# Kernel tuning notes

Measured on AMD Instinct MI355X. Metric: run time of the kernel, lower is better.

## Reference

```python
import jax, jax.numpy as jnp
import numpy as np

B, IN, H = 4096, 2048, 2048

def hard_sigmoid(x):
    # torch nn.Hardsigmoid / QHardSigmoid: clip(x/6 + 0.5, 0, 1)
    return jnp.clip(x / 6.0 + 0.5, 0.0, 1.0)

def hard_tanh(x):
    return jnp.clip(x, -1.0, 1.0)

def setup_inputs() -> dict:
    key = jax.random.key(0)
    k1, k2, k3, k4, k5 = jax.random.split(key, 5)
    return {
        "input_": jax.random.normal(k1, (B, IN), dtype=jnp.float32),
        "h_0": jax.random.normal(k2, (B, H), dtype=jnp.float32),
        "c_0": jax.random.normal(k3, (B, H), dtype=jnp.float32),
        "W_ih": jax.random.normal(k4, (4 * H, IN), dtype=jnp.float32) * (1.0 / np.sqrt(IN)),
        "W_hh": jax.random.normal(k5, (4 * H, H), dtype=jnp.float32) * (1.0 / np.sqrt(H)),
        "b_hh": jnp.zeros((4 * H,), dtype=jnp.float32),
    }

def reference(input_, h_0, c_0, W_ih, W_hh, b_hh):
    # Two GEMMs: x @ W_ih^T (no bias) and h @ W_hh^T + b
    wi = jnp.einsum('bi,gi->bg', input_, W_ih)          # [B, 4H]
    wh_b = jnp.einsum('bh,gh->bg', h_0, W_hh) + b_hh     # [B, 4H]
    h_x4 = wh_b + wi
    f, i, o, g = jnp.split(h_x4, 4, axis=1)              # split order: f, i, o, g
    new = hard_sigmoid(i) * hard_tanh(g)
    old = hard_sigmoid(f) * c_0
    c_1 = old + new
    h_1 = hard_sigmoid(o) * hard_tanh(c_1)
    return (h_1, c_1)
```

## Files before the change

kernel.cpp:

```cpp
#include <hip/hip_runtime.h>
#include <hip/hip_bf16.h>


typedef __attribute__((ext_vector_type(8))) short short8;
typedef __attribute__((ext_vector_type(4))) float f32x4;

#define B_SZ 4096
#define K_SZ 4096
#define N_SZ 8192
#define H_SZ 2048

typedef const __attribute__((address_space(1))) void gvoid_t;
typedef __attribute__((address_space(3))) void lvoid_t;

__device__ __forceinline__ void gload_lds16(const __hip_bfloat16* g, void* l) {
    __builtin_amdgcn_global_load_lds((gvoid_t*)g, (lvoid_t*)l, 16, 0, 0);
}

__device__ __forceinline__ float hsig(float x) {
    return fminf(fmaxf(x * (1.0f / 6.0f) + 0.5f, 0.0f), 1.0f);
}
__device__ __forceinline__ float htanh(float x) {
    return fminf(fmaxf(x, -1.0f), 1.0f);
}

__global__ void cvt_concat_kernel(const float* __restrict__ a,
                                  const float* __restrict__ b,
                                  __hip_bfloat16* __restrict__ out,
                                  int total4)
{
    int i = blockIdx.x * blockDim.x + threadIdx.x;
    if (i >= total4) return;
    int idx = i << 2;
    int r = idx >> 12;
    int c = idx & 4095;
    const float* src = (c < 2048) ? (a + (size_t)r * 2048 + c)
                                  : (b + (size_t)r * 2048 + (c - 2048));
    float4 v = *reinterpret_cast<const float4*>(src);
    union { ushort4 u; __hip_bfloat16 h[4]; } p;
    p.h[0] = __float2bfloat16(v.x);
    p.h[1] = __float2bfloat16(v.y);
    p.h[2] = __float2bfloat16(v.z);
    p.h[3] = __float2bfloat16(v.w);
    *reinterpret_cast<ushort4*>(out + idx) = p.u;
}

__global__ void cvt_w_perm_kernel(const float* __restrict__ wih,
                                  const float* __restrict__ whh,
                                  __hip_bfloat16* __restrict__ out,
                                  int total4)
{
    int i = blockIdx.x * blockDim.x + threadIdx.x;
    if (i >= total4) return;
    int idx = i << 2;
    int r = idx >> 12;
    int c = idx & 4095;
    int gate = (((r >> 7) & 1) << 1) | ((r >> 4) & 1);
    int j = (r & 15) | (((r >> 5) & 3) << 4) | ((r >> 8) << 6);
    int srow = gate * 2048 + j;
    const float* src = (c < 2048) ? (wih + (size_t)srow * 2048 + c)
                                  : (whh + (size_t)srow * 2048 + (c - 2048));
    float4 v = *reinterpret_cast<const float4*>(src);
    union { ushort4 u; __hip_bfloat16 h[4]; } p;
    p.h[0] = __float2bfloat16(v.x);
    p.h[1] = __float2bfloat16(v.y);
    p.h[2] = __float2bfloat16(v.z);
    p.h[3] = __float2bfloat16(v.w);
    *reinterpret_cast<ushort4*>(out + idx) = p.u;
}

__global__ __launch_bounds__(512, 2)
void gemm_fused_kernel(const __hip_bfloat16* __restrict__ A,
                       const __hip_bfloat16* __restrict__ Bw,
                       const float* __restrict__ c0,
                       const float* __restrict__ bias,
                       float* __restrict__ out)
{
    constexpr int BK = 64;
    constexpr int NT = K_SZ / BK;
    constexpr int NWG = (B_SZ / 256) * (N_SZ / 256);
    constexpr int TILEB = 65536;

    extern __shared__ __align__(16) char lds[];

    const int tid  = threadIdx.x;
    const int wave = tid >> 6;
    const int lane = tid & 63;
    const int wrow = wave >> 2;
    const int wcol = wave & 3;
    const int fr   = lane & 15;
    const int fkq  = lane >> 4;

    int bid = blockIdx.x;
    int swz = (bid & 7) * (NWG / 8) + (bid >> 3);
    int bm = swz >> 5;
    int bn = swz & 31;

    const int rs  = tid >> 3;
    const int ch  = tid & 7;
    const int lch = ch ^ (rs & 7);
    const __hip_bfloat16* pa = A  + (size_t)(bm * 256 + rs) * K_SZ + lch * 8;
    const __hip_bfloat16* pb = Bw + (size_t)(bn * 256 + rs) * K_SZ + lch * 8;

#define STG_A(bufn, kt, srow) \
    gload_lds16(pa + (size_t)(srow) * K_SZ + (kt), (bufn) + (srow) * 128 + wave * 1024)
#define STG_B(bufn, kt, srow) \
    gload_lds16(pb + (size_t)(srow) * K_SZ + (kt), (bufn) + 32768 + (srow) * 128 + wave * 1024)

    int a_off[4], b_off[2];
#pragma unroll
    for (int mf = 0; mf < 4; ++mf) {
        int row = wrow * 64 + mf * 16 + fr;
        a_off[mf] = row * 128 + ((fkq ^ (row & 7)) << 4);
    }
#pragma unroll
    for (int nf = 0; nf < 2; ++nf) {
        int row = wcol * 32 + nf * 16 + fr;
        b_off[nf] = row * 128 + ((fkq ^ (row & 7)) << 4);
    }

    f32x4 acc[8][4];
#pragma unroll
    for (int m = 0; m < 8; ++m)
#pragma unroll
        for (int n = 0; n < 4; ++n)
            acc[m][n] = f32x4{0.f, 0.f, 0.f, 0.f};

    {
        char* b0 = lds;
        STG_A(b0, 0, 0);   STG_A(b0, 0, 64);
        STG_B(b0, 0, 0);   STG_B(b0, 0, 64);
        STG_A(b0, 0, 128); STG_A(b0, 0, 192);
        STG_B(b0, 0, 128); STG_B(b0, 0, 192);
    }
    asm volatile("s_waitcnt vmcnt(4)" ::: "memory");
    asm volatile("s_barrier" ::: "memory");

    short8 av[4][2], bv[2][2];

#pragma unroll 1
    for (int t = 0; t < NT; ++t) {
        char* bufc = lds + (t & 1) * TILEB;
        char* bufn = lds + ((t + 1) & 1) * TILEB;
        const char* Ab = bufc;
        const char* Bb = bufc + 32768;
        const int ktn = (t + 1) * BK;
        const bool st = (t + 1 < NT);

#pragma unroll
        for (int mf = 0; mf < 4; ++mf)
#pragma unroll
            for (int ks = 0; ks < 2; ++ks)
                av[mf][ks] = *(const short8*)(Ab + (a_off[mf] ^ (ks << 6)));
#pragma unroll
        for (int nf = 0; nf < 2; ++nf)
#pragma unroll
            for (int ks = 0; ks < 2; ++ks)
                bv[nf][ks] = *(const short8*)(Bb + (b_off[nf] ^ (ks << 6)));
        if (st) { STG_A(bufn, ktn, 0); STG_A(bufn, ktn, 64); }
        asm volatile("s_barrier" ::: "memory");
        asm volatile("s_waitcnt lgkmcnt(0)" ::: "memory");
        __builtin_amdgcn_sched_barrier(0);
        __builtin_amdgcn_s_setprio(1);
#pragma unroll
        for (int mf = 0; mf < 4; ++mf)
#pragma unroll
            for (int nf = 0; nf < 2; ++nf)
#pragma unroll
                for (int ks = 0; ks < 2; ++ks)
                    acc[mf][nf] = __builtin_amdgcn_mfma_f32_16x16x32_bf16(av[mf][ks], bv[nf][ks], acc[mf][nf], 0, 0, 0);
        __builtin_amdgcn_s_setprio(0);
        if (st) asm volatile("s_waitcnt vmcnt(2)" ::: "memory");
        else    asm volatile("s_waitcnt vmcnt(0)" ::: "memory");
        asm volatile("s_barrier" ::: "memory");

#pragma unroll
        for (int nf = 0; nf < 2; ++nf)
#pragma unroll
            for (int ks = 0; ks < 2; ++ks)
                bv[nf][ks] = *(const short8*)(Bb + 16384 + (b_off[nf] ^ (ks << 6)));
        if (st) { STG_B(bufn, ktn, 0); STG_B(bufn, ktn, 64); }
        asm volatile("s_barrier" ::: "memory");
        asm volatile("s_waitcnt lgkmcnt(0)" ::: "memory");
        __builtin_amdgcn_sched_barrier(0);
        __builtin_amdgcn_s_setprio(1);
#pragma unroll
        for (int mf = 0; mf < 4; ++mf)
#pragma unroll
            for (int nf = 0; nf < 2; ++nf)
#pragma unroll
                for (int ks = 0; ks < 2; ++ks)
                    acc[mf][2 + nf] = __builtin_amdgcn_mfma_f32_16x16x32_bf16(av[mf][ks], bv[nf][ks], acc[mf][2 + nf], 0, 0, 0);
        __builtin_amdgcn_s_setprio(0);
        asm volatile("s_barrier" ::: "memory");

#pragma unroll
        for (int mf = 0; mf < 4; ++mf)
#pragma unroll
            for (int ks = 0; ks < 2; ++ks)
                av[mf][ks] = *(const short8*)(Ab + 16384 + (a_off[mf] ^ (ks << 6)));
#pragma unroll
        for (int nf = 0; nf < 2; ++nf)
#pragma unroll
            for (int ks = 0; ks < 2; ++ks)
                bv[nf][ks] = *(const short8*)(Bb + (b_off[nf] ^ (ks << 6)));
        if (st) { STG_A(bufn, ktn, 128); STG_A(bufn, ktn, 192); }
        asm volatile("s_barrier" ::: "memory");
        asm volatile("s_waitcnt lgkmcnt(0)" ::: "memory");
        __builtin_amdgcn_sched_barrier(0);
        __builtin_amdgcn_s_setprio(1);
#pragma unroll
        for (int mf = 0; mf < 4; ++mf)
#pragma unroll
            for (int nf = 0; nf < 2; ++nf)
#pragma unroll
                for (int ks = 0; ks < 2; ++ks)
                    acc[4 + mf][nf] = __builtin_amdgcn_mfma_f32_16x16x32_bf16(av[mf][ks], bv[nf][ks], acc[4 + mf][nf], 0, 0, 0);
        __builtin_amdgcn_s_setprio(0);
        asm volatile("s_barrier" ::: "memory");

#pragma unroll
        for (int nf = 0; nf < 2; ++nf)
#pragma unroll
            for (int ks = 0; ks < 2; ++ks)
                bv[nf][ks] = *(const short8*)(Bb + 16384 + (b_off[nf] ^ (ks << 6)));
        if (st) { STG_B(bufn, ktn, 128); STG_B(bufn, ktn, 192); }
        asm volatile("s_barrier" ::: "memory");
        asm volatile("s_waitcnt lgkmcnt(0)" ::: "memory");
        __builtin_amdgcn_sched_barrier(0);
        __builtin_amdgcn_s_setprio(1);
#pragma unroll
        for (int mf = 0; mf < 4; ++mf)
#pragma unroll
            for (int nf = 0; nf < 2; ++nf)
#pragma unroll
                for (int ks = 0; ks < 2; ++ks)
                    acc[4 + mf][2 + nf] = __builtin_amdgcn_mfma_f32_16x16x32_bf16(av[mf][ks], bv[nf][ks], acc[4 + mf][2 + nf], 0, 0, 0);
        __builtin_amdgcn_s_setprio(0);
        if (st) asm volatile("s_waitcnt vmcnt(4)" ::: "memory");
        asm volatile("s_barrier" ::: "memory");
    }
#undef STG_A
#undef STG_B

    const int jj = bn * 64 + wcol * 16 + fr;
    const float bf = bias[jj];
    const float bi = bias[2048 + jj];
    const float bo = bias[4096 + jj];
    const float bg = bias[6144 + jj];
    float* h1out = out;
    float* c1out = out + (size_t)B_SZ * H_SZ;
#pragma unroll
    for (int mh = 0; mh < 2; ++mh)
#pragma unroll
        for (int mf = 0; mf < 4; ++mf) {
            const int m = mh * 4 + mf;
            const int row0 = bm * 256 + mh * 128 + wrow * 64 + mf * 16 + fkq * 4;
#pragma unroll
            for (int i = 0; i < 4; ++i) {
                int r = row0 + i;
                float c0v = c0[(size_t)r * H_SZ + jj];
                float f  = acc[m][0][i] + bf;
                float ig = acc[m][1][i] + bi;
                float o  = acc[m][2][i] + bo;
                float g  = acc[m][3][i] + bg;
                float cn = hsig(f) * c0v + hsig(ig) * htanh(g);
                h1out[(size_t)r * H_SZ + jj] = hsig(o) * htanh(cn);
                c1out[(size_t)r * H_SZ + jj] = cn;
            }
        }
}

extern "C" void kernel_launch(void* const* d_in, const int* in_sizes, int n_in,
                              void* d_out, int out_size, void* d_ws, size_t ws_size,
                              hipStream_t stream)
{
    const float* x   = (const float*)d_in[0];
    const float* h0  = (const float*)d_in[1];
    const float* c0  = (const float*)d_in[2];
    const float* Wih = (const float*)d_in[3];
    const float* Whh = (const float*)d_in[4];
    const float* bhh = (const float*)d_in[5];
    float* out = (float*)d_out;

    if (ws_size < (size_t)96 * 1024 * 1024) return;
    char* ws = (char*)d_ws;
    __hip_bfloat16* Xp = (__hip_bfloat16*)ws;
    __hip_bfloat16* Wp = (__hip_bfloat16*)(ws + (size_t)32 * 1024 * 1024);

    int t4x = B_SZ * K_SZ / 4;
    cvt_concat_kernel<<<t4x / 256, 256, 0, stream>>>(x, h0, Xp, t4x);
    int t4w = N_SZ * K_SZ / 4;
    cvt_w_perm_kernel<<<t4w / 256, 256, 0, stream>>>(Wih, Whh, Wp, t4w);

    gemm_fused_kernel<<<512, 512, 131072, stream>>>(Xp, Wp, c0, bhh, out);
}
```

Before: 480.4 us.

## Keep both B sub-tiles in registers per k-step and widen bf16 conversion to 8 elements

The GEMM main loop now loads both halves of the B tile into separate register sets (bv0, bv1) once per k-step. It reuses them across the two A halves, so the repeated B reads from LDS go away and only one A reload remains. The global-to-LDS staging order and the vmcnt wait counts are rearranged to match, and some lgkmcnt waits are dropped. The conversion kernels now process 8 floats per thread with 16-byte stores. The extra B registers raise register pressure, and the loosened waits make correctness depend on the exact order of outstanding loads.

```diff
diff --git a/kernel.cpp b/kernel.cpp
--- a/kernel.cpp
+++ b/kernel.cpp
@@ -24,35 +24,40 @@
     return fminf(fmaxf(x, -1.0f), 1.0f);
 }
 
+__device__ __forceinline__ void cvt8_store(const float* src, __hip_bfloat16* dst) {
+    float4 v0 = *reinterpret_cast<const float4*>(src);
+    float4 v1 = *reinterpret_cast<const float4*>(src + 4);
+    union { __hip_bfloat16 h[8]; uint4 q; } p;
+    p.h[0] = __float2bfloat16(v0.x); p.h[1] = __float2bfloat16(v0.y);
+    p.h[2] = __float2bfloat16(v0.z); p.h[3] = __float2bfloat16(v0.w);
+    p.h[4] = __float2bfloat16(v1.x); p.h[5] = __float2bfloat16(v1.y);
+    p.h[6] = __float2bfloat16(v1.z); p.h[7] = __float2bfloat16(v1.w);
+    *reinterpret_cast<uint4*>(dst) = p.q;
+}
+
 __global__ void cvt_concat_kernel(const float* __restrict__ a,
                                   const float* __restrict__ b,
                                   __hip_bfloat16* __restrict__ out,
-                                  int total4)
+                                  int total8)
 {
     int i = blockIdx.x * blockDim.x + threadIdx.x;
-    if (i >= total4) return;
-    int idx = i << 2;
+    if (i >= total8) return;
+    int idx = i << 3;
     int r = idx >> 12;
     int c = idx & 4095;
     const float* src = (c < 2048) ? (a + (size_t)r * 2048 + c)
                                   : (b + (size_t)r * 2048 + (c - 2048));
-    float4 v = *reinterpret_cast<const float4*>(src);
-    union { ushort4 u; __hip_bfloat16 h[4]; } p;
-    p.h[0] = __float2bfloat16(v.x);
-    p.h[1] = __float2bfloat16(v.y);
-    p.h[2] = __float2bfloat16(v.z);
-    p.h[3] = __float2bfloat16(v.w);
-    *reinterpret_cast<ushort4*>(out + idx) = p.u;
+    cvt8_store(src, out + idx);
 }
 
 __global__ void cvt_w_perm_kernel(const float* __restrict__ wih,
                                   const float* __restrict__ whh,
                                   __hip_bfloat16* __restrict__ out,
-                                  int total4)
+                                  int total8)
 {
     int i = blockIdx.x * blockDim.x + threadIdx.x;
-    if (i >= total4) return;
-    int idx = i << 2;
+    if (i >= total8) return;
+    int idx = i << 3;
     int r = idx >> 12;
     int c = idx & 4095;
     int gate = (((r >> 7) & 1) << 1) | ((r >> 4) & 1);
@@ -60,13 +65,7 @@
     int srow = gate * 2048 + j;
     const float* src = (c < 2048) ? (wih + (size_t)srow * 2048 + c)
                                   : (whh + (size_t)srow * 2048 + (c - 2048));
-    float4 v = *reinterpret_cast<const float4*>(src);
-    union { ushort4 u; __hip_bfloat16 h[4]; } p;
-    p.h[0] = __float2bfloat16(v.x);
-    p.h[1] = __float2bfloat16(v.y);
-    p.h[2] = __float2bfloat16(v.z);
-    p.h[3] = __float2bfloat16(v.w);
-    *reinterpret_cast<ushort4*>(out + idx) = p.u;
+    cvt8_store(src, out + idx);
 }
 
 __global__ __launch_bounds__(512, 2)
@@ -130,13 +129,13 @@
         char* b0 = lds;
         STG_A(b0, 0, 0);   STG_A(b0, 0, 64);
         STG_B(b0, 0, 0);   STG_B(b0, 0, 64);
+        STG_B(b0, 0, 128); STG_B(b0, 0, 192);
         STG_A(b0, 0, 128); STG_A(b0, 0, 192);
-        STG_B(b0, 0, 128); STG_B(b0, 0, 192);
-    }
-    asm volatile("s_waitcnt vmcnt(4)" ::: "memory");
+    }
+    asm volatile("s_waitcnt vmcnt(2)" ::: "memory");
     asm volatile("s_barrier" ::: "memory");
 
-    short8 av[4][2], bv[2][2];
+    short8 av[4][2], bv0[2][2], bv1[2][2];
 
 #pragma unroll 1
     for (int t = 0; t < NT; ++t) {
@@ -155,8 +154,10 @@
 #pragma unroll
         for (int nf = 0; nf < 2; ++nf)
 #pragma unroll
-            for (int ks = 0; ks < 2; ++ks)
-                bv[nf][ks] = *(const short8*)(Bb + (b_off[nf] ^ (ks << 6)));
+            for (int ks = 0; ks < 2; ++ks) {
+                bv0[nf][ks] = *(const short8*)(Bb + (b_off[nf] ^ (ks << 6)));
+                bv1[nf][ks] = *(const short8*)(Bb + 16384 + (b_off[nf] ^ (ks << 6)));
+            }
         if (st) { STG_A(bufn, ktn, 0); STG_A(bufn, ktn, 64); }
         asm volatile("s_barrier" ::: "memory");
         asm volatile("s_waitcnt lgkmcnt(0)" ::: "memory");
@@ -168,18 +169,31 @@
             for (int nf = 0; nf < 2; ++nf)
 #pragma unroll
                 for (int ks = 0; ks < 2; ++ks)
-                    acc[mf][nf] = __builtin_amdgcn_mfma_f32_16x16x32_bf16(av[mf][ks], bv[nf][ks], acc[mf][nf], 0, 0, 0);
-        __builtin_amdgcn_s_setprio(0);
-        if (st) asm volatile("s_waitcnt vmcnt(2)" ::: "memory");
+                    acc[mf][nf] = __builtin_amdgcn_mfma_f32_16x16x32_bf16(av[mf][ks], bv0[nf][ks], acc[mf][nf], 0, 0, 0);
+        __builtin_amdgcn_s_setprio(0);
+        asm volatile("s_barrier" ::: "memory");
+
+        if (st) { STG_B(bufn, ktn, 0); STG_B(bufn, ktn, 64); }
+        asm volatile("s_barrier" ::: "memory");
+        __builtin_amdgcn_s_setprio(1);
+#pragma unroll
+        for (int mf = 0; mf < 4; ++mf)
+#pragma unroll
+            for (int nf = 0; nf < 2; ++nf)
+#pragma unroll
+                for (int ks = 0; ks < 2; ++ks)
+                    acc[mf][2 + nf] = __builtin_amdgcn_mfma_f32_16x16x32_bf16(av[mf][ks], bv1[nf][ks], acc[mf][2 + nf], 0, 0, 0);
+        __builtin_amdgcn_s_setprio(0);
+        if (st) asm volatile("s_waitcnt vmcnt(4)" ::: "memory");
         else    asm volatile("s_waitcnt vmcnt(0)" ::: "memory");
         asm volatile("s_barrier" ::: "memory");
 
 #pragma unroll
-        for (int nf = 0; nf < 2; ++nf)
+        for (int mf = 0; mf < 4; ++mf)
 #pragma unroll
             for (int ks = 0; ks < 2; ++ks)
-                bv[nf][ks] = *(const short8*)(Bb + 16384 + (b_off[nf] ^ (ks << 6)));
-        if (st) { STG_B(bufn, ktn, 0); STG_B(bufn, ktn, 64); }
+                av[mf][ks] = *(const short8*)(Ab + 16384 + (a_off[mf] ^ (ks << 6)));
+        if (st) { STG_B(bufn, ktn, 128); STG_B(bufn, ktn, 192); }
         asm volatile("s_barrier" ::: "memory");
         asm volatile("s_waitcnt lgkmcnt(0)" ::: "memory");
         __builtin_amdgcn_sched_barrier(0);
@@ -190,54 +204,22 @@
             for (int nf = 0; nf < 2; ++nf)
 #pragma unroll
                 for (int ks = 0; ks < 2; ++ks)
-                    acc[mf][2 + nf] = __builtin_amdgcn_mfma_f32_16x16x32_bf16(av[mf][ks], bv[nf][ks], acc[mf][2 + nf], 0, 0, 0);
-        __builtin_amdgcn_s_setprio(0);
-        asm volatile("s_barrier" ::: "memory");
-
-#pragma unroll
-        for (int mf = 0; mf < 4; ++mf)
-#pragma unroll
-            for (int ks = 0; ks < 2; ++ks)
-                av[mf][ks] = *(const short8*)(Ab + 16384 + (a_off[mf] ^ (ks << 6)));
-#pragma unroll
-        for (int nf = 0; nf < 2; ++nf)
-#pragma unroll
-            for (int ks = 0; ks < 2; ++ks)
-                bv[nf][ks] = *(const short8*)(Bb + (b_off[nf] ^ (ks << 6)));
+                    acc[4 + mf][nf] = __builtin_amdgcn_mfma_f32_16x16x32_bf16(av[mf][ks], bv0[nf][ks], acc[4 + mf][nf], 0, 0, 0);
+        __builtin_amdgcn_s_setprio(0);
+        asm volatile("s_barrier" ::: "memory");
+
         if (st) { STG_A(bufn, ktn, 128); STG_A(bufn, ktn, 192); }
         asm volatile("s_barrier" ::: "memory");
-        asm volatile("s_waitcnt lgkmcnt(0)" ::: "memory");
-        __builtin_amdgcn_sched_barrier(0);
-        __builtin_amdgcn_s_setprio(1);
-#pragma unroll
-        for (int mf = 0; mf < 4; ++mf)
-#pragma unroll
-            for (int nf = 0; nf < 2; ++nf)
-#pragma unroll
-                for (int ks = 0; ks < 2; ++ks)
-                    acc[4 + mf][nf] = __builtin_amdgcn_mfma_f32_16x16x32_bf16(av[mf][ks], bv[nf][ks], acc[4 + mf][nf], 0, 0, 0);
-        __builtin_amdgcn_s_setprio(0);
-        asm volatile("s_barrier" ::: "memory");
-
-#pragma unroll
-        for (int nf = 0; nf < 2; ++nf)
-#pragma unroll
-            for (int ks = 0; ks < 2; ++ks)
-                bv[nf][ks] = *(const short8*)(Bb + 16384 + (b_off[nf] ^ (ks << 6)));
-        if (st) { STG_B(bufn, ktn, 128); STG_B(bufn, ktn, 192); }
-        asm volatile("s_barrier" ::: "memory");
-        asm volatile("s_waitcnt lgkmcnt(0)" ::: "memory");
-        __builtin_amdgcn_sched_barrier(0);
-        __builtin_amdgcn_s_setprio(1);
-#pragma unroll
-        for (int mf = 0; mf < 4; ++mf)
-#pragma unroll
-            for (int nf = 0; nf < 2; ++nf)
-#pragma unroll
-                for (int ks = 0; ks < 2; ++ks)
-                    acc[4 + mf][2 + nf] = __builtin_amdgcn_mfma_f32_16x16x32_bf16(av[mf][ks], bv[nf][ks], acc[4 + mf][2 + nf], 0, 0, 0);
-        __builtin_amdgcn_s_setprio(0);
-        if (st) asm volatile("s_waitcnt vmcnt(4)" ::: "memory");
+        __builtin_amdgcn_s_setprio(1);
+#pragma unroll
+        for (int mf = 0; mf < 4; ++mf)
+#pragma unroll
+            for (int nf = 0; nf < 2; ++nf)
+#pragma unroll
+                for (int ks = 0; ks < 2; ++ks)
+                    acc[4 + mf][2 + nf] = __builtin_amdgcn_mfma_f32_16x16x32_bf16(av[mf][ks], bv1[nf][ks], acc[4 + mf][2 + nf], 0, 0, 0);
+        __builtin_amdgcn_s_setprio(0);
+        if (st) asm volatile("s_waitcnt vmcnt(2)" ::: "memory");
         asm volatile("s_barrier" ::: "memory");
     }
 #undef STG_A
@@ -288,10 +270,10 @@
     __hip_bfloat16* Xp = (__hip_bfloat16*)ws;
     __hip_bfloat16* Wp = (__hip_bfloat16*)(ws + (size_t)32 * 1024 * 1024);
 
-    int t4x = B_SZ * K_SZ / 4;
-    cvt_concat_kernel<<<t4x / 256, 256, 0, stream>>>(x, h0, Xp, t4x);
-    int t4w = N_SZ * K_SZ / 4;
-    cvt_w_perm_kernel<<<t4w / 256, 256, 0, stream>>>(Wih, Whh, Wp, t4w);
+    int t8x = B_SZ * K_SZ / 8;
+    cvt_concat_kernel<<<t8x / 256, 256, 0, stream>>>(x, h0, Xp, t8x);
+    int t8w = N_SZ * K_SZ / 8;
+    cvt_w_perm_kernel<<<t8w / 256, 256, 0, stream>>>(Wih, Whh, Wp, t8w);
 
     gemm_fused_kernel<<<512, 512, 131072, stream>>>(Xp, Wp, c0, bhh, out);
 }
```

Measured after the change: 467.2 us. 2.7% less time.
